# Performance work log

Hardware: AMD Instinct MI355X
Metric: run time of the kernel (lower is better)

## Reference

```python
import jax, jax.numpy as jnp
from jax import lax
import numpy as np

KSIZE = 3  # dynamic depthwise kernel size
DN = ('NCHW', 'OIHW', 'NCHW')


def setup_inputs() -> dict:
    key = jax.random.key(0)
    ks = jax.random.split(key, 6)
    B, C, H, W = 16, 64, 192, 192
    x = jax.random.normal(ks[0], (B, C, H, W), dtype=jnp.float32)
    k_v = jax.random.normal(ks[1], (B, 64), dtype=jnp.float32)
    # kernel-generating MLP (torch nn.Linear weights, y = x @ W.T), scaled for stability
    W1 = jax.random.normal(ks[2], (64, 64), dtype=jnp.float32) * (1.0 / np.sqrt(64))
    W2 = jax.random.normal(ks[3], (C * KSIZE * KSIZE, 64), dtype=jnp.float32) * (1.0 / np.sqrt(64))
    # static Conv2d(C, C, 3, padding=1)
    conv_w = jax.random.normal(ks[4], (C, C, 3, 3), dtype=jnp.float32) * (1.0 / np.sqrt(C * 9))
    conv_b = jax.random.normal(ks[5], (C,), dtype=jnp.float32) * 0.01
    return {"x": x, "k_v": k_v, "W1": W1, "W2": W2, "conv_w": conv_w, "conv_b": conv_b}


def reference(x, k_v, W1, W2, conv_w, conv_b):
    b, c, h, w = x.shape
    pad = (KSIZE - 1) // 2
    # kernel = Linear -> LeakyReLU(0.1) -> Linear, viewed as (b*c, 1, k, k)
    hid = jax.nn.leaky_relu(k_v @ W1.T, negative_slope=0.1)            # (b, 64)
    kern = (hid @ W2.T).reshape(b * c, 1, KSIZE, KSIZE)                # (b*c, 1, k, k)
    # grouped depthwise conv: one distinct kxk kernel per (batch, channel)
    out = lax.conv_general_dilated(
        x.reshape(1, b * c, h, w), kern,
        window_strides=(1, 1), padding=[(pad, pad), (pad, pad)],
        feature_group_count=b * c, dimension_numbers=DN)
    out = jax.nn.leaky_relu(out, negative_slope=0.1).reshape(b, c, h, w)
    # static 3x3 conv residual branch
    res = lax.conv_general_dilated(
        x, conv_w, window_strides=(1, 1), padding=[(1, 1), (1, 1)],
        dimension_numbers=DN) + conv_b[None, :, None, None]
    return out + res
```

## Files before the change

### kernel.cpp

```cpp
#include <hip/hip_runtime.h>
#include <hip/hip_bf16.h>

#define B_ 16
#define C_ 64
#define H_ 192
#define W_ 192

#define TR 4
#define TC 48
#define PCH 72

typedef short bf16x8 __attribute__((ext_vector_type(8)));
typedef float f32x4  __attribute__((ext_vector_type(4)));

static __device__ __forceinline__ unsigned short f2bf(float f) {
    union { float f; unsigned u; } v; v.f = f;
    unsigned r = v.u + 0x7fff + ((v.u >> 16) & 1);
    return (unsigned short)(r >> 16);
}
static __device__ __forceinline__ float bf2f(unsigned short u) {
    union { unsigned u; float f; } v; v.u = ((unsigned)u) << 16; return v.f;
}

__global__ void kgen(const float* __restrict__ k_v, const float* __restrict__ W1,
                     const float* __restrict__ W2, float* __restrict__ kern) {
    int b = blockIdx.x, c = threadIdx.x;
    __shared__ float kv[64], hid[64];
    kv[c] = k_v[b * 64 + c];
    __syncthreads();
    float s = 0.f;
#pragma unroll
    for (int k = 0; k < 64; ++k) s += kv[k] * W1[c * 64 + k];
    hid[c] = s > 0.f ? s : 0.1f * s;
    __syncthreads();
    for (int j = 0; j < 9; ++j) {
        int o = c * 9 + j;
        float t = 0.f;
#pragma unroll
        for (int k = 0; k < 64; ++k) t += hid[k] * W2[o * 64 + k];
        kern[b * 576 + o] = t;
    }
}

__global__ void wtrans(const float* __restrict__ conv_w, unsigned short* __restrict__ wT) {
    int idx = blockIdx.x * 256 + threadIdx.x;
    int tap = idx >> 12;
    int rem = idx & 4095;
    int n = rem >> 6;
    int k = rem & 63;
    wT[idx] = f2bf(conv_w[(n * 64 + k) * 9 + tap]);
}

__global__ __launch_bounds__(256, 3)
void fused_conv(const float* __restrict__ x, const unsigned short* __restrict__ wT,
                const float* __restrict__ kern, const float* __restrict__ conv_b,
                float* __restrict__ out) {
    const int bx = blockIdx.x;
    const int by = blockIdx.y;
    const int b  = blockIdx.z;
    const int tid  = threadIdx.x;
    const int lane = tid & 63;
    const int wv   = tid >> 6;
    const int n0   = lane & 15;
    const int q    = lane >> 4;

    const int r0 = by * TR;
    const int c0 = bx * TC;

    __shared__ __align__(16) unsigned short smem[6 * 50 * PCH + 64 * PCH];
    unsigned short* xs = smem;
    unsigned short* bs = smem + 6 * 50 * PCH;

    for (int i = tid; i < 6 * 50 * 64; i += 256) {
        int ch = i / 300;
        int rc = i % 300;
        int r = rc / 50, c = rc % 50;
        int gr = r0 + r - 1, gc = c0 + c - 1;
        float v = 0.f;
        if (gr >= 0 && gr < H_ && gc >= 0 && gc < W_)
            v = x[((b * C_ + ch) * H_ + gr) * W_ + gc];
        xs[(r * 50 + c) * PCH + ch] = f2bf(v);
    }

    f32x4 acc[3][4];
#pragma unroll
    for (int i = 0; i < 3; ++i)
#pragma unroll
        for (int j = 0; j < 4; ++j) acc[i][j] = (f32x4){0.f, 0.f, 0.f, 0.f};

    for (int tap = 0; tap < 9; ++tap) {
        __syncthreads();
        {
            int n  = tid >> 2;
            int kb = (tid & 3) * 16;
            const unsigned short* src = wT + tap * 4096 + n * 64 + kb;
            *(bf16x8*)(bs + n * PCH + kb)     = *(const bf16x8*)(src);
            *(bf16x8*)(bs + n * PCH + kb + 8) = *(const bf16x8*)(src + 8);
        }
        __syncthreads();
        const int dr = tap / 3, dc = tap % 3;

        bf16x8 bf[4][2];
#pragma unroll
        for (int nt = 0; nt < 4; ++nt)
#pragma unroll
            for (int ks = 0; ks < 2; ++ks)
                bf[nt][ks] = *(const bf16x8*)(bs + (nt * 16 + n0) * PCH + ks * 32 + q * 8);

#pragma unroll
        for (int cb = 0; cb < 3; ++cb) {
            const int col = cb * 16 + n0 + dc;
            const int row = wv + dr;
            const unsigned short* ap = xs + (row * 50 + col) * PCH + q * 8;
            bf16x8 a0 = *(const bf16x8*)(ap);
            bf16x8 a1 = *(const bf16x8*)(ap + 32);
#pragma unroll
            for (int nt = 0; nt < 4; ++nt) {
                acc[cb][nt] = __builtin_amdgcn_mfma_f32_16x16x32_bf16(a0, bf[nt][0], acc[cb][nt], 0, 0, 0);
                acc[cb][nt] = __builtin_amdgcn_mfma_f32_16x16x32_bf16(a1, bf[nt][1], acc[cb][nt], 0, 0, 0);
            }
        }
    }

    __syncthreads();
    float* kf = (float*)(smem + 6 * 50 * PCH);
    for (int i = tid; i < 640; i += 256)
        kf[i] = (i < 576) ? kern[b * 576 + i] : conv_b[i - 576];
    __syncthreads();

#pragma unroll
    for (int nt = 0; nt < 4; ++nt) {
        const int n = nt * 16 + n0;
        float kw[9];
#pragma unroll
        for (int j = 0; j < 9; ++j) kw[j] = kf[n * 9 + j];
        const float bias = kf[576 + n];
#pragma unroll
        for (int cb = 0; cb < 3; ++cb) {
            const int colb = cb * 16 + q * 4;
            float xw[3][6];
#pragma unroll
            for (int d = 0; d < 3; ++d)
#pragma unroll
                for (int cc = 0; cc < 6; ++cc)
                    xw[d][cc] = bf2f(xs[((wv + d) * 50 + colb + cc) * PCH + n]);
            float4 st;
#pragma unroll
            for (int r = 0; r < 4; ++r) {
                float dw = 0.f;
#pragma unroll
                for (int d = 0; d < 3; ++d)
#pragma unroll
                    for (int e = 0; e < 3; ++e)
                        dw += kw[d * 3 + e] * xw[d][r + e];
                float v = (dw > 0.f ? dw : 0.1f * dw) + acc[cb][nt][r] + bias;
                ((float*)&st)[r] = v;
            }
            float* op = out + ((b * C_ + n) * H_ + (r0 + wv)) * W_ + c0 + colb;
            *(float4*)op = st;
        }
    }
}

extern "C" void kernel_launch(void* const* d_in, const int* in_sizes, int n_in,
                              void* d_out, int out_size, void* d_ws, size_t ws_size,
                              hipStream_t stream) {
    const float* x      = (const float*)d_in[0];
    const float* k_v    = (const float*)d_in[1];
    const float* W1     = (const float*)d_in[2];
    const float* W2     = (const float*)d_in[3];
    const float* conv_w = (const float*)d_in[4];
    const float* conv_b = (const float*)d_in[5];
    float* outp = (float*)d_out;

    float* kern        = (float*)d_ws;
    unsigned short* wT = (unsigned short*)((char*)d_ws + 40960);

    kgen<<<16, 64, 0, stream>>>(k_v, W1, W2, kern);
    wtrans<<<144, 256, 0, stream>>>(conv_w, wT);
    dim3 grid(4, 48, 16);
    fused_conv<<<grid, 256, 0, stream>>>(x, wT, kern, conv_b, outp);
}
```

Before: 459.1 us.

## Vectorize x tile load, XOR-swizzle LDS, read weights from global, split kgen

The halo tile of x is now loaded as float4 across 8 channels at once and stored as packed bf16x8 into an XOR-swizzled, unpadded LDS layout, replacing the scalar strided gather. Per-tap weight staging through LDS and its two barriers per tap are removed; B fragments are read directly from global/L2, as are the dynamic kernel and bias in the epilogue. The kernel-generating MLP is split into two kernels so the second layer runs across 36 blocks instead of 16 serial loops. The cost is more global/L2 traffic for weights inside the MFMA loop.

After: 418.0 us. 1.1x faster.

```diff
diff --git a/kernel.cpp b/kernel.cpp
--- a/kernel.cpp
+++ b/kernel.cpp
@@ -1,14 +1,11 @@
 #include <hip/hip_runtime.h>
-#include <hip/hip_bf16.h>
 
 #define B_ 16
 #define C_ 64
 #define H_ 192
 #define W_ 192
-
 #define TR 4
 #define TC 48
-#define PCH 72
 
 typedef short bf16x8 __attribute__((ext_vector_type(8)));
 typedef float f32x4  __attribute__((ext_vector_type(4)));
@@ -21,33 +18,39 @@
 static __device__ __forceinline__ float bf2f(unsigned short u) {
     union { unsigned u; float f; } v; v.u = ((unsigned)u) << 16; return v.f;
 }
-
-__global__ void kgen(const float* __restrict__ k_v, const float* __restrict__ W1,
-                     const float* __restrict__ W2, float* __restrict__ kern) {
+static __device__ __forceinline__ int xsw(int p, int ch) {
+    return p * 64 + (((ch >> 3) ^ (p & 7)) << 3) + (ch & 7);
+}
+
+__global__ void kgen1(const float* __restrict__ k_v, const float* __restrict__ W1,
+                      float* __restrict__ hid) {
     int b = blockIdx.x, c = threadIdx.x;
-    __shared__ float kv[64], hid[64];
+    __shared__ float kv[64];
     kv[c] = k_v[b * 64 + c];
     __syncthreads();
     float s = 0.f;
 #pragma unroll
     for (int k = 0; k < 64; ++k) s += kv[k] * W1[c * 64 + k];
-    hid[c] = s > 0.f ? s : 0.1f * s;
-    __syncthreads();
-    for (int j = 0; j < 9; ++j) {
-        int o = c * 9 + j;
-        float t = 0.f;
-#pragma unroll
-        for (int k = 0; k < 64; ++k) t += hid[k] * W2[o * 64 + k];
-        kern[b * 576 + o] = t;
-    }
+    hid[b * 64 + c] = s > 0.f ? s : 0.1f * s;
+}
+
+__global__ void kgen2(const float* __restrict__ hid, const float* __restrict__ W2,
+                      float* __restrict__ kern) {
+    int idx = blockIdx.x * 256 + threadIdx.x;
+    int b = idx / 576, o = idx - b * 576;
+    const float* h = hid + b * 64;
+    const float* w = W2 + o * 64;
+    float t = 0.f;
+#pragma unroll
+    for (int k = 0; k < 64; ++k) t += h[k] * w[k];
+    kern[idx] = t;
 }
 
 __global__ void wtrans(const float* __restrict__ conv_w, unsigned short* __restrict__ wT) {
     int idx = blockIdx.x * 256 + threadIdx.x;
     int tap = idx >> 12;
     int rem = idx & 4095;
-    int n = rem >> 6;
-    int k = rem & 63;
+    int n = rem >> 6, k = rem & 63;
     wT[idx] = f2bf(conv_w[(n * 64 + k) * 9 + tap]);
 }
 
@@ -63,23 +66,48 @@
     const int wv   = tid >> 6;
     const int n0   = lane & 15;
     const int q    = lane >> 4;
-
     const int r0 = by * TR;
     const int c0 = bx * TC;
 
-    __shared__ __align__(16) unsigned short smem[6 * 50 * PCH + 64 * PCH];
-    unsigned short* xs = smem;
-    unsigned short* bs = smem + 6 * 50 * PCH;
-
-    for (int i = tid; i < 6 * 50 * 64; i += 256) {
-        int ch = i / 300;
-        int rc = i % 300;
-        int r = rc / 50, c = rc % 50;
-        int gr = r0 + r - 1, gc = c0 + c - 1;
-        float v = 0.f;
-        if (gr >= 0 && gr < H_ && gc >= 0 && gc < W_)
-            v = x[((b * C_ + ch) * H_ + gr) * W_ + gc];
-        xs[(r * 50 + c) * PCH + ch] = f2bf(v);
+    __shared__ __align__(16) unsigned short xs[6 * 50 * 64];
+
+    for (int u = tid; u < 576; u += 256) {
+        int chg  = u / 72;
+        int rest = u - chg * 72;
+        int row  = rest / 12;
+        int cg   = rest - row * 12;
+        int gr   = r0 + row - 1;
+        bool in  = (gr >= 0 && gr < H_);
+        int grc  = in ? gr : 0;
+        const float* xp = x + ((size_t)(b * 64 + chg * 8) * H_ + grc) * W_ + c0 + cg * 4;
+        float4 f[8];
+#pragma unroll
+        for (int j = 0; j < 8; ++j)
+            f[j] = in ? *(const float4*)(xp + j * H_ * W_) : make_float4(0.f, 0.f, 0.f, 0.f);
+#pragma unroll
+        for (int e = 0; e < 4; ++e) {
+            int p = row * 50 + 1 + cg * 4 + e;
+            union { bf16x8 v; unsigned short s[8]; } wv8;
+#pragma unroll
+            for (int j = 0; j < 8; ++j) wv8.s[j] = f2bf(((const float*)&f[j])[e]);
+            *(bf16x8*)(xs + xsw(p, chg * 8)) = wv8.v;
+        }
+    }
+    if (tid < 96) {
+        int chg  = tid / 12;
+        int rest = tid - chg * 12;
+        int row  = rest >> 1;
+        int sc   = (rest & 1) ? 49 : 0;
+        int gr = r0 + row - 1, gc = c0 + sc - 1;
+        bool in = (gr >= 0 && gr < H_ && gc >= 0 && gc < W_);
+        union { bf16x8 v; unsigned short s[8]; } wv8;
+#pragma unroll
+        for (int j = 0; j < 8; ++j) {
+            float vv = 0.f;
+            if (in) vv = x[((size_t)(b * 64 + chg * 8 + j) * H_ + gr) * W_ + gc];
+            wv8.s[j] = f2bf(vv);
+        }
+        *(bf16x8*)(xs + xsw(row * 50 + sc, chg * 8)) = wv8.v;
     }
 
     f32x4 acc[3][4];
@@ -88,32 +116,22 @@
 #pragma unroll
         for (int j = 0; j < 4; ++j) acc[i][j] = (f32x4){0.f, 0.f, 0.f, 0.f};
 
+    __syncthreads();
+
+#pragma unroll
     for (int tap = 0; tap < 9; ++tap) {
-        __syncthreads();
-        {
-            int n  = tid >> 2;
-            int kb = (tid & 3) * 16;
-            const unsigned short* src = wT + tap * 4096 + n * 64 + kb;
-            *(bf16x8*)(bs + n * PCH + kb)     = *(const bf16x8*)(src);
-            *(bf16x8*)(bs + n * PCH + kb + 8) = *(const bf16x8*)(src + 8);
-        }
-        __syncthreads();
         const int dr = tap / 3, dc = tap % 3;
-
         bf16x8 bf[4][2];
 #pragma unroll
         for (int nt = 0; nt < 4; ++nt)
 #pragma unroll
             for (int ks = 0; ks < 2; ++ks)
-                bf[nt][ks] = *(const bf16x8*)(bs + (nt * 16 + n0) * PCH + ks * 32 + q * 8);
-
+                bf[nt][ks] = *(const bf16x8*)(wT + tap * 4096 + (nt * 16 + n0) * 64 + ks * 32 + q * 8);
 #pragma unroll
         for (int cb = 0; cb < 3; ++cb) {
-            const int col = cb * 16 + n0 + dc;
-            const int row = wv + dr;
-            const unsigned short* ap = xs + (row * 50 + col) * PCH + q * 8;
-            bf16x8 a0 = *(const bf16x8*)(ap);
-            bf16x8 a1 = *(const bf16x8*)(ap + 32);
+            const int p = (wv + dr) * 50 + cb * 16 + n0 + dc;
+            bf16x8 a0 = *(const bf16x8*)(xs + p * 64 + ((q ^ (p & 7)) << 3));
+            bf16x8 a1 = *(const bf16x8*)(xs + p * 64 + (((q + 4) ^ (p & 7)) << 3));
 #pragma unroll
             for (int nt = 0; nt < 4; ++nt) {
                 acc[cb][nt] = __builtin_amdgcn_mfma_f32_16x16x32_bf16(a0, bf[nt][0], acc[cb][nt], 0, 0, 0);
@@ -122,19 +140,15 @@
         }
     }
 
-    __syncthreads();
-    float* kf = (float*)(smem + 6 * 50 * PCH);
-    for (int i = tid; i < 640; i += 256)
-        kf[i] = (i < 576) ? kern[b * 576 + i] : conv_b[i - 576];
-    __syncthreads();
-
+    const float* kp = kern + b * 576;
 #pragma unroll
     for (int nt = 0; nt < 4; ++nt) {
         const int n = nt * 16 + n0;
         float kw[9];
 #pragma unroll
-        for (int j = 0; j < 9; ++j) kw[j] = kf[n * 9 + j];
-        const float bias = kf[576 + n];
+        for (int j = 0; j < 9; ++j) kw[j] = kp[n * 9 + j];
+        const float bias = conv_b[n];
+        const int gn = n >> 3, n7 = n & 7;
 #pragma unroll
         for (int cb = 0; cb < 3; ++cb) {
             const int colb = cb * 16 + q * 4;
@@ -142,8 +156,10 @@
 #pragma unroll
             for (int d = 0; d < 3; ++d)
 #pragma unroll
-                for (int cc = 0; cc < 6; ++cc)
-                    xw[d][cc] = bf2f(xs[((wv + d) * 50 + colb + cc) * PCH + n]);
+                for (int cc = 0; cc < 6; ++cc) {
+                    int p = (wv + d) * 50 + colb + cc;
+                    xw[d][cc] = bf2f(xs[p * 64 + ((gn ^ (p & 7)) << 3) + n7]);
+                }
             float4 st;
 #pragma unroll
             for (int r = 0; r < 4; ++r) {
@@ -156,8 +172,7 @@
                 float v = (dw > 0.f ? dw : 0.1f * dw) + acc[cb][nt][r] + bias;
                 ((float*)&st)[r] = v;
             }
-            float* op = out + ((b * C_ + n) * H_ + (r0 + wv)) * W_ + c0 + colb;
-            *(float4*)op = st;
+            *(float4*)(out + ((size_t)(b * 64 + n) * H_ + (r0 + wv)) * W_ + c0 + colb) = st;
         }
     }
 }
@@ -175,8 +190,10 @@
 
     float* kern        = (float*)d_ws;
     unsigned short* wT = (unsigned short*)((char*)d_ws + 40960);
-
-    kgen<<<16, 64, 0, stream>>>(k_v, W1, W2, kern);
+    float* hid         = (float*)((char*)d_ws + 114688);
+
+    kgen1<<<16, 64, 0, stream>>>(k_v, W1, hid);
+    kgen2<<<36, 256, 0, stream>>>(hid, W2, kern);
     wtrans<<<144, 256, 0, stream>>>(conv_w, wT);
     dim3 grid(4, 48, 16);
     fused_conv<<<grid, 256, 0, stream>>>(x, wT, kern, conv_b, outp);
```
